# Performance work log

Measured on AMD Instinct MI355X. Metric: run time of the kernel, lower is better.

Reference implementation:

```python
import jax, jax.numpy as jnp
import numpy as np

DIM = 1024          # BIGNET_DIM
LORA = 32
GROUP = 128
N_LIN = 18          # 6 blocks * 3 QLoRALinear
N_LN = 5
EPS = 1e-5


def setup_inputs() -> dict:
    key = jax.random.key(0)
    ks = jax.random.split(key, 8)
    tokens = 16384
    x = jax.random.normal(ks[0], (tokens, DIM), dtype=jnp.float32)
    # int4 codes in [0,16), per-(out,group) scale (block-abs-max norm)
    q = jax.random.randint(ks[1], (N_LIN, DIM, DIM), 0, 16, dtype=jnp.int32)
    norm = jax.random.uniform(ks[2], (N_LIN, DIM, DIM // GROUP), dtype=jnp.float32) * 0.1 + 0.01
    bias = jax.random.normal(ks[3], (N_LIN, DIM), dtype=jnp.float32) * 0.01
    # lora_a: kaiming-uniform * 0.01; lora_b: zeros in the original init, but we use
    # small random values so the LoRA path (and its gradients) are exercised.
    lora_a = jax.random.normal(ks[4], (N_LIN, LORA, DIM), dtype=jnp.float32) * 0.01
    lora_b = jax.random.normal(ks[5], (N_LIN, DIM, LORA), dtype=jnp.float32) * 0.01
    ln_gamma = jnp.ones((N_LN, DIM), dtype=jnp.float32)
    ln_beta = jnp.zeros((N_LN, DIM), dtype=jnp.float32)
    return {"x": x, "q": q, "norm": norm, "bias": bias,
            "lora_a": lora_a, "lora_b": lora_b,
            "ln_gamma": ln_gamma, "ln_beta": ln_beta}


def _dequant(qi, ni):
    # qi: [O, I] int codes in [0,16); ni: [O, I//GROUP] group scales
    O, I = qi.shape
    w = (qi.astype(jnp.float32) / 15.0 * 2.0 - 1.0).reshape(O, I // GROUP, GROUP)
    return (w * ni[..., None]).reshape(O, I)


def _qlora_linear(h, qi, ni, b, la, lb):
    w = _dequant(qi, ni)                      # [O, I]
    base = h @ w.T + b                        # frozen quantized path
    lora = (h @ la.T) @ lb.T                  # rank-32 adapter
    return base + lora


def _layernorm(h, g, b):
    mu = jnp.mean(h, axis=-1, keepdims=True)
    var = jnp.var(h, axis=-1, keepdims=True)
    return (h - mu) * jax.lax.rsqrt(var + EPS) * g + b


def _forward(x, q, norm, bias, lora_a, lora_b, ln_gamma, ln_beta):
    h = x
    for blk in range(6):
        r = h
        for j in range(3):
            i = 3 * blk + j
            r = _qlora_linear(r, q[i], norm[i], bias[i], lora_a[i], lora_b[i])
            if j < 2:
                r = jax.nn.relu(r)
        h = r + h                              # residual
        if blk < 5:
            h = _layernorm(h, ln_gamma[blk], ln_beta[blk])
    return h


def reference(x, q, norm, bias, lora_a, lora_b, ln_gamma, ln_beta):
    return _forward(x, q, norm, bias, lora_a, lora_b, ln_gamma, ln_beta)
```

## Files before the change

kernel.cpp:

```cpp
#include <hip/hip_runtime.h>
#include <stdint.h>


#define TOK   16384
#define DIM   1024
#define NLIN  18
#define EPS   1e-5f

typedef _Float16 f16;
typedef _Float16 f16x8 __attribute__((ext_vector_type(8)));
typedef _Float16 f16x4 __attribute__((ext_vector_type(4)));
typedef float    f32x4 __attribute__((ext_vector_type(4)));

__device__ __forceinline__ void load_lds16(const void* g, void* l) {
  __builtin_amdgcn_global_load_lds(
      (const __attribute__((address_space(1))) void*)g,
      (__attribute__((address_space(3))) void*)l,
      16, 0, 0);
}

__global__ __launch_bounds__(256) void prep_weights(
    const int* __restrict__ q, const float* __restrict__ norm,
    const float* __restrict__ la, const float* __restrict__ lb,
    f16* __restrict__ W)
{
  const int bid = blockIdx.x;
  const int i = bid >> 10;
  const int k4 = threadIdx.x * 4;
  const int4 qv = *(const int4*)(q + ((size_t)bid << 10) + k4);
  const float nrm = norm[bid * 8 + (k4 >> 7)];
  const float* lbr = lb + (size_t)bid * 32;
  const float* lal = la + (size_t)i * 32 * 1024 + k4;
  float ax = 0.f, ay = 0.f, az = 0.f, aw = 0.f;
  #pragma unroll
  for (int r = 0; r < 32; ++r) {
    const float b = lbr[r];
    const float4 a = *(const float4*)(lal + r * 1024);
    ax += b * a.x; ay += b * a.y; az += b * a.z; aw += b * a.w;
  }
  const float s = 2.f / 15.f;
  f16x4 hv;
  hv[0] = (f16)(((float)qv.x * s - 1.f) * nrm + ax);
  hv[1] = (f16)(((float)qv.y * s - 1.f) * nrm + ay);
  hv[2] = (f16)(((float)qv.z * s - 1.f) * nrm + az);
  hv[3] = (f16)(((float)qv.w * s - 1.f) * nrm + aw);
  *(f16x4*)(W + ((size_t)bid << 10) + k4) = hv;
}

__global__ __launch_bounds__(256) void cvt_x(
    const float* __restrict__ x, f16* __restrict__ o)
{
  const size_t idx = ((size_t)blockIdx.x * 256 + threadIdx.x) * 4;
  const float4 v = *(const float4*)(x + idx);
  f16x4 h;
  h[0] = (f16)v.x; h[1] = (f16)v.y; h[2] = (f16)v.z; h[3] = (f16)v.w;
  *(f16x4*)(o + idx) = h;
}

template<int EPI>
__global__ __launch_bounds__(256) void gemm_ql(
    const f16* __restrict__ A, const f16* __restrict__ W,
    const float* __restrict__ bias, const f16* __restrict__ resid,
    void* __restrict__ outp)
{
  __shared__ __align__(16) f16 sA[128 * 64];
  __shared__ __align__(16) f16 sB[128 * 64];

  const int orig = blockIdx.x;
  const int swzb = (orig & 7) * 128 + (orig >> 3);
  const int mt = swzb >> 3, nt = swzb & 7;
  const int t0 = mt * 128, n0 = nt * 128;

  const int tid  = threadIdx.x;
  const int lane = tid & 63;
  const int wid  = tid >> 6;
  const int wm = wid >> 1, wn = wid & 1;

  const int rb = tid >> 3;
  const int gc = (tid & 7) ^ (rb & 7);
  const f16* gA = A + (size_t)(t0 + rb) * DIM + gc * 8;
  const f16* gB = W + (size_t)(n0 + rb) * DIM + gc * 8;
  const int ldst = tid * 16;

  f32x4 acc[4][4] = {};

  int aoff[2][4], boff[2][4];
  #pragma unroll
  for (int kk = 0; kk < 2; ++kk) {
    const int kbyte = kk * 64 + ((lane >> 4) << 4);
    #pragma unroll
    for (int f = 0; f < 4; ++f) {
      const int ra = wm * 64 + f * 16 + (lane & 15);
      aoff[kk][f] = ra * 128 + (kbyte ^ ((ra & 7) << 4));
      const int rn = wn * 64 + f * 16 + (lane & 15);
      boff[kk][f] = rn * 128 + (kbyte ^ ((rn & 7) << 4));
    }
  }

  for (int kt = 0; kt < DIM / 64; ++kt) {
    const f16* a_src = gA + kt * 64;
    const f16* b_src = gB + kt * 64;
    #pragma unroll
    for (int qq = 0; qq < 4; ++qq) {
      load_lds16(a_src + (size_t)qq * 32 * DIM, (char*)sA + qq * 4096 + ldst);
      load_lds16(b_src + (size_t)qq * 32 * DIM, (char*)sB + qq * 4096 + ldst);
    }
    __syncthreads();
    #pragma unroll
    for (int kk = 0; kk < 2; ++kk) {
      f16x8 af[4], bf[4];
      #pragma unroll
      for (int f = 0; f < 4; ++f)
        af[f] = *(const f16x8*)((const char*)sA + aoff[kk][f]);
      #pragma unroll
      for (int f = 0; f < 4; ++f)
        bf[f] = *(const f16x8*)((const char*)sB + boff[kk][f]);
      #pragma unroll
      for (int mi = 0; mi < 4; ++mi)
        #pragma unroll
        for (int ni = 0; ni < 4; ++ni)
          acc[mi][ni] = __builtin_amdgcn_mfma_f32_16x16x32_f16(
              af[mi], bf[ni], acc[mi][ni], 0, 0, 0);
    }
    __syncthreads();
  }

  const int colb = lane & 15;
  const int rowb = (lane >> 4) << 2;
  #pragma unroll
  for (int ni = 0; ni < 4; ++ni) {
    const int col = n0 + wn * 64 + ni * 16 + colb;
    const float bv = bias[col];
    #pragma unroll
    for (int mi = 0; mi < 4; ++mi) {
      const int trow = t0 + wm * 64 + mi * 16 + rowb;
      const f32x4 v = acc[mi][ni];
      #pragma unroll
      for (int r = 0; r < 4; ++r) {
        const size_t idx = (size_t)(trow + r) * DIM + col;
        float val = v[r] + bv;
        if constexpr (EPI == 0) {
          val = fmaxf(val, 0.f);
          ((f16*)outp)[idx] = (f16)val;
        } else if constexpr (EPI == 1) {
          val += (float)resid[idx];
          ((f16*)outp)[idx] = (f16)val;
        } else {
          val += (float)resid[idx];
          ((float*)outp)[idx] = val;
        }
      }
    }
  }
}

__global__ __launch_bounds__(256) void ln_k(
    const f16* __restrict__ in, f16* __restrict__ out,
    const float* __restrict__ g, const float* __restrict__ b)
{
  __shared__ float red[8];
  const int row = blockIdx.x;
  const int tid = threadIdx.x;
  const int c = tid * 4;
  const f16x4 v4 = *(const f16x4*)(in + (size_t)row * DIM + c);
  const float v0 = v4[0], v1 = v4[1], v2 = v4[2], v3 = v4[3];
  float s  = v0 + v1 + v2 + v3;
  float s2 = v0 * v0 + v1 * v1 + v2 * v2 + v3 * v3;
  #pragma unroll
  for (int off = 32; off; off >>= 1) {
    s  += __shfl_xor(s,  off);
    s2 += __shfl_xor(s2, off);
  }
  if ((tid & 63) == 0) { red[(tid >> 6) * 2] = s; red[(tid >> 6) * 2 + 1] = s2; }
  __syncthreads();
  s  = red[0] + red[2] + red[4] + red[6];
  s2 = red[1] + red[3] + red[5] + red[7];
  const float mu  = s * (1.f / DIM);
  const float var = fmaxf(s2 * (1.f / DIM) - mu * mu, 0.f);
  const float rs  = rsqrtf(var + EPS);
  const float4 gv = *(const float4*)(g + c);
  const float4 bv = *(const float4*)(b + c);
  f16x4 o4;
  o4[0] = (f16)((v0 - mu) * rs * gv.x + bv.x);
  o4[1] = (f16)((v1 - mu) * rs * gv.y + bv.y);
  o4[2] = (f16)((v2 - mu) * rs * gv.z + bv.z);
  o4[3] = (f16)((v3 - mu) * rs * gv.w + bv.w);
  *(f16x4*)(out + (size_t)row * DIM + c) = o4;
}

extern "C" void kernel_launch(void* const* d_in, const int* in_sizes, int n_in,
                              void* d_out, int out_size, void* d_ws, size_t ws_size,
                              hipStream_t stream)
{
  (void)in_sizes; (void)n_in; (void)out_size; (void)ws_size;
  const float* x     = (const float*)d_in[0];
  const int*   q     = (const int*)d_in[1];
  const float* norm  = (const float*)d_in[2];
  const float* bias  = (const float*)d_in[3];
  const float* la    = (const float*)d_in[4];
  const float* lb    = (const float*)d_in[5];
  const float* lg    = (const float*)d_in[6];
  const float* lbeta = (const float*)d_in[7];

  char* ws = (char*)d_ws;
  f16* W    = (f16*)ws;
  f16* buf1 = (f16*)(ws + (size_t)NLIN * DIM * DIM * 2);
  f16* buf2 = buf1 + (size_t)TOK * DIM;
  f16* buf0 = (f16*)d_out;
  f16* bufs[3] = {buf0, buf1, buf2};

  prep_weights<<<NLIN * DIM, 256, 0, stream>>>(q, norm, la, lb, W);
  cvt_x<<<TOK * DIM / 1024, 256, 0, stream>>>(x, buf0);

  int h = 0;
  for (int blk = 0; blk < 6; ++blk) {
    const int a = (h == 0) ? 1 : 0;
    const int p = 3 - h - a;
    const int i0 = blk * 3;
    const size_t wsz = (size_t)DIM * DIM;
    gemm_ql<0><<<1024, 256, 0, stream>>>(bufs[h], W + (i0 + 0) * wsz,
                                         bias + (i0 + 0) * DIM, nullptr, bufs[a]);
    gemm_ql<0><<<1024, 256, 0, stream>>>(bufs[a], W + (i0 + 1) * wsz,
                                         bias + (i0 + 1) * DIM, nullptr, bufs[p]);
    if (blk < 5) {
      gemm_ql<1><<<1024, 256, 0, stream>>>(bufs[p], W + (i0 + 2) * wsz,
                                           bias + (i0 + 2) * DIM, bufs[h], bufs[a]);
      ln_k<<<TOK, 256, 0, stream>>>(bufs[a], bufs[a], lg + blk * DIM, lbeta + blk * DIM);
      h = a;
    } else {
      gemm_ql<2><<<1024, 256, 0, stream>>>(bufs[p], W + (i0 + 2) * wsz,
                                           bias + (i0 + 2) * DIM, bufs[h], d_out);
    }
  }
}
```

Baseline: 1.172 ms.

## Use 256x256 GEMM tiles with 4-stage LDS pipeline and tiled weight prep

The GEMM moves to 256x256 output tiles with 512 threads and a 4-buffer LDS ring (K step 32). Global-to-LDS loads are issued three stages ahead and gated with explicit vmcnt waits and a single barrier per step, plus setprio around the MFMA block. This is meant to hide memory latency and raise data reuse per tile. The weight-prep kernel now keeps lora_a in registers and lora_b in LDS, so each block computes a 128x256 tile instead of reloading the LoRA factors for every output row. Risks are that only 256 blocks run per GEMM on a large GPU, which may leave CUs idle, and that the heavy register use may cause spills.

```diff
diff --git a/kernel.cpp b/kernel.cpp
--- a/kernel.cpp
+++ b/kernel.cpp
@@ -19,32 +19,52 @@
       16, 0, 0);
 }
 
-__global__ __launch_bounds__(256) void prep_weights(
+__global__ __launch_bounds__(256) void prep_w2(
     const int* __restrict__ q, const float* __restrict__ norm,
     const float* __restrict__ la, const float* __restrict__ lb,
     f16* __restrict__ W)
 {
-  const int bid = blockIdx.x;
-  const int i = bid >> 10;
-  const int k4 = threadIdx.x * 4;
-  const int4 qv = *(const int4*)(q + ((size_t)bid << 10) + k4);
-  const float nrm = norm[bid * 8 + (k4 >> 7)];
-  const float* lbr = lb + (size_t)bid * 32;
-  const float* lal = la + (size_t)i * 32 * 1024 + k4;
-  float ax = 0.f, ay = 0.f, az = 0.f, aw = 0.f;
-  #pragma unroll
-  for (int r = 0; r < 32; ++r) {
-    const float b = lbr[r];
-    const float4 a = *(const float4*)(lal + r * 1024);
-    ax += b * a.x; ay += b * a.y; az += b * a.z; aw += b * a.w;
-  }
+  __shared__ float lbs[128 * 32];
+  const int bid   = blockIdx.x;
+  const int i     = bid >> 5;
+  const int ot    = (bid >> 2) & 7;
+  const int ktile = bid & 3;
+  const int o0 = ot * 128, k0 = ktile * 256;
+  const int tid = threadIdx.x;
+  const int kg = tid & 63, og = tid >> 6;
+  const int k4 = k0 + kg * 4;
+
+  const float* lbsrc = lb + (size_t)i * DIM * 32 + (size_t)o0 * 32;
+  #pragma unroll
+  for (int p = 0; p < 4; ++p)
+    *(float4*)(lbs + p * 1024 + tid * 4) = *(const float4*)(lbsrc + p * 1024 + tid * 4);
+
+  float4 lar[32];
+  const float* lasrc = la + (size_t)i * 32 * DIM + k4;
+  #pragma unroll
+  for (int r = 0; r < 32; ++r) lar[r] = *(const float4*)(lasrc + r * DIM);
+  __syncthreads();
+
   const float s = 2.f / 15.f;
-  f16x4 hv;
-  hv[0] = (f16)(((float)qv.x * s - 1.f) * nrm + ax);
-  hv[1] = (f16)(((float)qv.y * s - 1.f) * nrm + ay);
-  hv[2] = (f16)(((float)qv.z * s - 1.f) * nrm + az);
-  hv[3] = (f16)(((float)qv.w * s - 1.f) * nrm + aw);
-  *(f16x4*)(W + ((size_t)bid << 10) + k4) = hv;
+  for (int oi = 0; oi < 32; ++oi) {
+    const int o = o0 + og * 32 + oi;
+    const size_t wb = ((size_t)i * DIM + o) * DIM;
+    const int4 qv = *(const int4*)(q + wb + k4);
+    const float nrm = norm[((size_t)i * DIM + o) * 8 + (k4 >> 7)];
+    const float* lbr = lbs + (og * 32 + oi) * 32;
+    float ax = 0.f, ay = 0.f, az = 0.f, aw = 0.f;
+    #pragma unroll
+    for (int r = 0; r < 32; ++r) {
+      const float b = lbr[r];
+      ax += b * lar[r].x; ay += b * lar[r].y; az += b * lar[r].z; aw += b * lar[r].w;
+    }
+    f16x4 hv;
+    hv[0] = (f16)(((float)qv.x * s - 1.f) * nrm + ax);
+    hv[1] = (f16)(((float)qv.y * s - 1.f) * nrm + ay);
+    hv[2] = (f16)(((float)qv.z * s - 1.f) * nrm + az);
+    hv[3] = (f16)(((float)qv.w * s - 1.f) * nrm + aw);
+    *(f16x4*)(W + wb + k4) = hv;
+  }
 }
 
 __global__ __launch_bounds__(256) void cvt_x(
@@ -58,72 +78,83 @@
 }
 
 template<int EPI>
-__global__ __launch_bounds__(256) void gemm_ql(
+__global__ __launch_bounds__(512, 2) void gemm2(
     const f16* __restrict__ A, const f16* __restrict__ W,
     const float* __restrict__ bias, const f16* __restrict__ resid,
     void* __restrict__ outp)
 {
-  __shared__ __align__(16) f16 sA[128 * 64];
-  __shared__ __align__(16) f16 sB[128 * 64];
+  __shared__ __align__(16) char smem[131072];
 
   const int orig = blockIdx.x;
-  const int swzb = (orig & 7) * 128 + (orig >> 3);
-  const int mt = swzb >> 3, nt = swzb & 7;
-  const int t0 = mt * 128, n0 = nt * 128;
+  const int swzb = (orig & 7) * 32 + (orig >> 3);
+  const int mt = swzb >> 2, nt = swzb & 3;
+  const int t0 = mt * 256, n0 = nt * 256;
 
   const int tid  = threadIdx.x;
   const int lane = tid & 63;
   const int wid  = tid >> 6;
-  const int wm = wid >> 1, wn = wid & 1;
-
-  const int rb = tid >> 3;
-  const int gc = (tid & 7) ^ (rb & 7);
-  const f16* gA = A + (size_t)(t0 + rb) * DIM + gc * 8;
-  const f16* gB = W + (size_t)(n0 + rb) * DIM + gc * 8;
-  const int ldst = tid * 16;
-
-  f32x4 acc[4][4] = {};
-
-  int aoff[2][4], boff[2][4];
-  #pragma unroll
-  for (int kk = 0; kk < 2; ++kk) {
-    const int kbyte = kk * 64 + ((lane >> 4) << 4);
-    #pragma unroll
-    for (int f = 0; f < 4; ++f) {
-      const int ra = wm * 64 + f * 16 + (lane & 15);
-      aoff[kk][f] = ra * 128 + (kbyte ^ ((ra & 7) << 4));
-      const int rn = wn * 64 + f * 16 + (lane & 15);
-      boff[kk][f] = rn * 128 + (kbyte ^ ((rn & 7) << 4));
-    }
-  }
-
-  for (int kt = 0; kt < DIM / 64; ++kt) {
-    const f16* a_src = gA + kt * 64;
-    const f16* b_src = gB + kt * 64;
-    #pragma unroll
-    for (int qq = 0; qq < 4; ++qq) {
-      load_lds16(a_src + (size_t)qq * 32 * DIM, (char*)sA + qq * 4096 + ldst);
-      load_lds16(b_src + (size_t)qq * 32 * DIM, (char*)sB + qq * 4096 + ldst);
-    }
-    __syncthreads();
-    #pragma unroll
-    for (int kk = 0; kk < 2; ++kk) {
-      f16x8 af[4], bf[4];
+  const int wm = wid >> 2, wn = wid & 3;
+
+  const int srow   = tid >> 2;
+  const int schunk = (tid & 3) ^ ((tid >> 3) & 3);
+  const f16* gA = A + (size_t)(t0 + srow) * DIM + schunk * 8;
+  const f16* gB = W + (size_t)(n0 + srow) * DIM + schunk * 8;
+  const int sdst = tid * 16;
+
+  const int kchunk = ((lane >> 4) ^ ((lane >> 1) & 3)) * 16;
+  int aoff[8], boff[4];
+  #pragma unroll
+  for (int mi = 0; mi < 8; ++mi)
+    aoff[mi] = (wm * 128 + mi * 16 + (lane & 15)) * 64 + kchunk;
+  #pragma unroll
+  for (int ni = 0; ni < 4; ++ni)
+    boff[ni] = 16384 + (wn * 64 + ni * 16 + (lane & 15)) * 64 + kchunk;
+
+  f32x4 acc[8][4] = {};
+
+  auto stage = [&](int kt, int b) {
+    const f16* as = gA + kt * 32;
+    const f16* bs = gB + kt * 32;
+    char* d = smem + b * 32768 + sdst;
+    load_lds16(as, d);
+    load_lds16(as + (size_t)128 * DIM, d + 8192);
+    load_lds16(bs, d + 16384);
+    load_lds16(bs + (size_t)128 * DIM, d + 24576);
+  };
+  auto body = [&](int b) {
+    const char* base = smem + b * 32768;
+    f16x8 af[8], bf[4];
+    #pragma unroll
+    for (int ni = 0; ni < 4; ++ni) bf[ni] = *(const f16x8*)(base + boff[ni]);
+    #pragma unroll
+    for (int mi = 0; mi < 8; ++mi) af[mi] = *(const f16x8*)(base + aoff[mi]);
+    __builtin_amdgcn_s_setprio(1);
+    #pragma unroll
+    for (int mi = 0; mi < 8; ++mi)
       #pragma unroll
-      for (int f = 0; f < 4; ++f)
-        af[f] = *(const f16x8*)((const char*)sA + aoff[kk][f]);
-      #pragma unroll
-      for (int f = 0; f < 4; ++f)
-        bf[f] = *(const f16x8*)((const char*)sB + boff[kk][f]);
-      #pragma unroll
-      for (int mi = 0; mi < 4; ++mi)
-        #pragma unroll
-        for (int ni = 0; ni < 4; ++ni)
-          acc[mi][ni] = __builtin_amdgcn_mfma_f32_16x16x32_f16(
-              af[mi], bf[ni], acc[mi][ni], 0, 0, 0);
-    }
-    __syncthreads();
-  }
+      for (int ni = 0; ni < 4; ++ni)
+        acc[mi][ni] = __builtin_amdgcn_mfma_f32_16x16x32_f16(
+            af[mi], bf[ni], acc[mi][ni], 0, 0, 0);
+    __builtin_amdgcn_s_setprio(0);
+  };
+
+  stage(0, 0); stage(1, 1); stage(2, 2);
+
+  for (int t = 0; t < 30; ++t) {
+    asm volatile("s_waitcnt vmcnt(8)" ::: "memory");
+    __builtin_amdgcn_s_barrier();
+    __builtin_amdgcn_sched_barrier(0);
+    if (t < 29) stage(t + 3, (t + 3) & 3);
+    body(t & 3);
+  }
+  asm volatile("s_waitcnt vmcnt(4)" ::: "memory");
+  __builtin_amdgcn_s_barrier();
+  __builtin_amdgcn_sched_barrier(0);
+  body(2);
+  asm volatile("s_waitcnt vmcnt(0)" ::: "memory");
+  __builtin_amdgcn_s_barrier();
+  __builtin_amdgcn_sched_barrier(0);
+  body(3);
 
   const int colb = lane & 15;
   const int rowb = (lane >> 4) << 2;
@@ -132,8 +163,8 @@
     const int col = n0 + wn * 64 + ni * 16 + colb;
     const float bv = bias[col];
     #pragma unroll
-    for (int mi = 0; mi < 4; ++mi) {
-      const int trow = t0 + wm * 64 + mi * 16 + rowb;
+    for (int mi = 0; mi < 8; ++mi) {
+      const int trow = t0 + wm * 128 + mi * 16 + rowb;
       const f32x4 v = acc[mi][ni];
       #pragma unroll
       for (int r = 0; r < 4; ++r) {
@@ -209,7 +240,7 @@
   f16* buf0 = (f16*)d_out;
   f16* bufs[3] = {buf0, buf1, buf2};
 
-  prep_weights<<<NLIN * DIM, 256, 0, stream>>>(q, norm, la, lb, W);
+  prep_w2<<<NLIN * 32, 256, 0, stream>>>(q, norm, la, lb, W);
   cvt_x<<<TOK * DIM / 1024, 256, 0, stream>>>(x, buf0);
 
   int h = 0;
@@ -218,18 +249,18 @@
     const int p = 3 - h - a;
     const int i0 = blk * 3;
     const size_t wsz = (size_t)DIM * DIM;
-    gemm_ql<0><<<1024, 256, 0, stream>>>(bufs[h], W + (i0 + 0) * wsz,
-                                         bias + (i0 + 0) * DIM, nullptr, bufs[a]);
-    gemm_ql<0><<<1024, 256, 0, stream>>>(bufs[a], W + (i0 + 1) * wsz,
-                                         bias + (i0 + 1) * DIM, nullptr, bufs[p]);
+    gemm2<0><<<256, 512, 0, stream>>>(bufs[h], W + (i0 + 0) * wsz,
+                                      bias + (i0 + 0) * DIM, nullptr, bufs[a]);
+    gemm2<0><<<256, 512, 0, stream>>>(bufs[a], W + (i0 + 1) * wsz,
+                                      bias + (i0 + 1) * DIM, nullptr, bufs[p]);
     if (blk < 5) {
-      gemm_ql<1><<<1024, 256, 0, stream>>>(bufs[p], W + (i0 + 2) * wsz,
-                                           bias + (i0 + 2) * DIM, bufs[h], bufs[a]);
+      gemm2<1><<<256, 512, 0, stream>>>(bufs[p], W + (i0 + 2) * wsz,
+                                        bias + (i0 + 2) * DIM, bufs[h], bufs[a]);
       ln_k<<<TOK, 256, 0, stream>>>(bufs[a], bufs[a], lg + blk * DIM, lbeta + blk * DIM);
       h = a;
     } else {
-      gemm_ql<2><<<1024, 256, 0, stream>>>(bufs[p], W + (i0 + 2) * wsz,
-                                           bias + (i0 + 2) * DIM, bufs[h], d_out);
+      gemm2<2><<<256, 512, 0, stream>>>(bufs[p], W + (i0 + 2) * wsz,
+                                        bias + (i0 + 2) * DIM, bufs[h], d_out);
     }
   }
 }
```

New measurement: 1.045 ms. -10.8%, faster.
